# Optimization experiments

Measured on AMD Instinct MI355X. Metric: run time of the kernel, lower is better.

The kernel has to match this reference:

```python
import jax, jax.numpy as jnp
import numpy as np

IN_FEATURES = 4096
OUT_FEATURES = 4096
ACTIVE_IN = 1024
ACTIVE_OUT = 1024
BATCH, SEQ = 4, 2048


def setup_inputs() -> dict:
    key = jax.random.key(0)
    kx, kw, kb = jax.random.split(key, 3)
    x = jax.random.normal(kx, (BATCH, SEQ, IN_FEATURES), dtype=jnp.float32)
    # nn.Linear default init scale ~ 1/sqrt(fan_in)
    W = jax.random.normal(kw, (ACTIVE_OUT, ACTIVE_IN), dtype=jnp.float32) / np.sqrt(ACTIVE_IN)
    b = jax.random.normal(kb, (ACTIVE_OUT,), dtype=jnp.float32) / np.sqrt(ACTIVE_IN)
    rng = np.random.default_rng(42)
    # unique sorted index subsets (faithful to pruning-style selection; scatter is write-once)
    in_idx = jnp.asarray(np.sort(rng.choice(IN_FEATURES, ACTIVE_IN, replace=False)), dtype=jnp.int32)
    out_idx = jnp.asarray(np.sort(rng.choice(OUT_FEATURES, ACTIVE_OUT, replace=False)), dtype=jnp.int32)
    return {"x": x, "W": W, "b": b, "in_idx": in_idx, "out_idx": out_idx}


def reference(x, W, b, in_idx, out_idx):
    # gather active input columns: [B, S, ACTIVE_IN]
    x_active = jnp.take(x, in_idx, axis=-1)
    # dense linear: y = x_active @ W.T + b -> [B, S, ACTIVE_OUT]
    y = jnp.einsum('bsi,oi->bso', x_active, W) + b
    # scatter into zero-initialized full output buffer: [B, S, OUT_FEATURES]
    out = jnp.zeros(x.shape[:-1] + (OUT_FEATURES,), dtype=y.dtype)
    out = out.at[..., out_idx].set(y)
    return out
```

## Files before the change

### kernel.cpp

```cpp
#include <hip/hip_runtime.h>
#include <hip/hip_bf16.h>


typedef unsigned short u16;
typedef u16   u16x4 __attribute__((ext_vector_type(4)));
typedef int   i32x4 __attribute__((ext_vector_type(4)));
typedef float f32x4 __attribute__((ext_vector_type(4)));
typedef __bf16 bf16x8 __attribute__((ext_vector_type(8)));

constexpr int IN_F  = 4096;
constexpr int OUT_F = 4096;
constexpr int AI    = 1024;
constexpr int AO    = 1024;
constexpr int M_ROWS = 4 * 2048;

__device__ __forceinline__ u16 f2bf(float f) {
    union { __hip_bfloat16 h; u16 u; } cv;
    cv.h = __float2bfloat16(f);
    return cv.u;
}
__device__ __forceinline__ float bf2f(u16 u) {
    union { float f; unsigned int i; } cv;
    cv.i = ((unsigned int)u) << 16;
    return cv.f;
}

__global__ void prep_kernel(const float* __restrict__ W,
                            const int* __restrict__ out_idx,
                            u16* __restrict__ Wb, int* __restrict__ pos) {
    int t = blockIdx.x * blockDim.x + threadIdx.x;
    if (t < AO) pos[out_idx[t]] = t;
    f32x4 w = reinterpret_cast<const f32x4*>(W)[t];
    u16x4 v;
    v.x = f2bf(w.x); v.y = f2bf(w.y); v.z = f2bf(w.z); v.w = f2bf(w.w);
    reinterpret_cast<u16x4*>(Wb)[t] = v;
}

__global__ __launch_bounds__(256)
void gather_kernel(const float* __restrict__ x,
                   const int* __restrict__ in_idx,
                   u16* __restrict__ Xa) {
    __shared__ float xrow[IN_F];
    const int m = blockIdx.x;
    const int t = threadIdx.x;
    const f32x4* src = reinterpret_cast<const f32x4*>(x + (size_t)m * IN_F);
#pragma unroll
    for (int i = 0; i < 4; ++i)
        *reinterpret_cast<f32x4*>(&xrow[i * 1024 + t * 4]) = src[i * 256 + t];
    __syncthreads();
    i32x4 idx = reinterpret_cast<const i32x4*>(in_idx)[t];
    u16x4 v;
    v.x = f2bf(xrow[idx.x]);
    v.y = f2bf(xrow[idx.y]);
    v.z = f2bf(xrow[idx.z]);
    v.w = f2bf(xrow[idx.w]);
    reinterpret_cast<u16x4*>(Xa + (size_t)m * AI)[t] = v;
}

__global__ __launch_bounds__(256, 2)
void gemmfw_kernel(const u16* __restrict__ Xa, const u16* __restrict__ Wb,
                   const float* __restrict__ bias,
                   const int* __restrict__ out_idx,
                   const int* __restrict__ pos, float* __restrict__ out) {
    __shared__ u16 S[4][128 * 64];
    const int t    = threadIdx.x;
    const int wid  = t >> 6;
    const int lane = t & 63;
    const int n_lo = lane & 15;
    const int kg   = lane >> 4;
    const int orig = blockIdx.x;
    const int wgid = (orig & 7) * 64 + (orig >> 3);
    const int mb = wgid >> 3, nb = wgid & 7;
    const int m0 = mb * 128, n0 = nb * 128;
    const int wm = wid >> 1, wn = wid & 1;

    const int r8 = lane >> 3;
    const int c8 = (lane & 7) * 8;
    auto stage = [&](int buf, int k0) {
#pragma unroll
        for (int c = 0; c < 4; ++c) {
            const int row = wid * 32 + c * 8;
            __builtin_amdgcn_global_load_lds(
                (const __attribute__((address_space(1))) void*)
                    (Xa + (size_t)(m0 + row + r8) * AI + k0 + c8),
                (__attribute__((address_space(3))) void*)&S[buf][row * 64],
                16, 0, 0);
            __builtin_amdgcn_global_load_lds(
                (const __attribute__((address_space(1))) void*)
                    (Wb + (size_t)(n0 + row + r8) * AI + k0 + c8),
                (__attribute__((address_space(3))) void*)&S[2 + buf][row * 64],
                16, 0, 0);
        }
    };

    f32x4 acc[4][4];
#pragma unroll
    for (int i = 0; i < 4; ++i)
#pragma unroll
        for (int j = 0; j < 4; ++j) acc[i][j] = (f32x4)0.0f;

    stage(0, 0);
    int buf = 0;
    for (int kt = 0; kt < AI / 64; ++kt) {
        __syncthreads();
        if (kt + 1 < AI / 64) stage(buf ^ 1, (kt + 1) * 64);
#pragma unroll
        for (int kk = 0; kk < 64; kk += 32) {
            bf16x8 a[4], b[4];
#pragma unroll
            for (int i = 0; i < 4; ++i)
                a[i] = *reinterpret_cast<const bf16x8*>(
                    &S[buf][(wm * 64 + i * 16 + n_lo) * 64 + kk + kg * 8]);
#pragma unroll
            for (int j = 0; j < 4; ++j)
                b[j] = *reinterpret_cast<const bf16x8*>(
                    &S[2 + buf][(wn * 64 + j * 16 + n_lo) * 64 + kk + kg * 8]);
#pragma unroll
            for (int i = 0; i < 4; ++i)
#pragma unroll
                for (int j = 0; j < 4; ++j)
                    acc[i][j] = __builtin_amdgcn_mfma_f32_16x16x32_bf16(
                        a[i], b[j], acc[i][j], 0, 0, 0);
        }
        buf ^= 1;
    }

    float bv[4];
#pragma unroll
    for (int j = 0; j < 4; ++j) bv[j] = bias[n0 + wn * 64 + j * 16 + n_lo];

    __syncthreads();
    u16* ys = &S[0][0];
#pragma unroll
    for (int i = 0; i < 4; ++i)
#pragma unroll
        for (int j = 0; j < 4; ++j)
#pragma unroll
            for (int r = 0; r < 4; ++r)
                ys[(wm * 64 + i * 16 + kg * 4 + r) * 136 +
                   wn * 64 + j * 16 + n_lo] = f2bf(acc[i][j][r] + bv[j]);
    __syncthreads();

    const int lo = (nb == 0) ? 0 : out_idx[nb * 128];
    const int hi = (nb == 7) ? OUT_F : out_idx[(nb + 1) * 128];
    const int s4 = (lo + 3) >> 2;
    const int e4 = hi >> 2;
    const i32x4* pos4 = reinterpret_cast<const i32x4*>(pos);
    const int rg = t >> 5, j32 = t & 31;
#pragma unroll 1
    for (int rr = 0; rr < 128; rr += 8) {
        const int row = rr + rg;
        float* orow = out + (size_t)(m0 + row) * OUT_F;
        const u16* yr = ys + row * 136;
        for (int c = lo + j32; c < s4 * 4; c += 32) {
            int p = pos[c];
            orow[c] = (p >= 0) ? bf2f(yr[p - n0]) : 0.0f;
        }
        for (int c4 = s4 + j32; c4 < e4; c4 += 32) {
            i32x4 p = pos4[c4];
            f32x4 v;
            v.x = (p.x >= 0) ? bf2f(yr[p.x - n0]) : 0.0f;
            v.y = (p.y >= 0) ? bf2f(yr[p.y - n0]) : 0.0f;
            v.z = (p.z >= 0) ? bf2f(yr[p.z - n0]) : 0.0f;
            v.w = (p.w >= 0) ? bf2f(yr[p.w - n0]) : 0.0f;
            reinterpret_cast<f32x4*>(orow)[c4] = v;
        }
        for (int c = e4 * 4 + j32; c < hi; c += 32) {
            int p = pos[c];
            orow[c] = (p >= 0) ? bf2f(yr[p - n0]) : 0.0f;
        }
    }
}

extern "C" void kernel_launch(void* const* d_in, const int* in_sizes, int n_in,
                              void* d_out, int out_size, void* d_ws, size_t ws_size,
                              hipStream_t stream) {
    const float* x      = (const float*)d_in[0];
    const float* W      = (const float*)d_in[1];
    const float* b      = (const float*)d_in[2];
    const int*   in_idx = (const int*)d_in[3];
    const int*   out_idx= (const int*)d_in[4];
    float* out = (float*)d_out;

    char* ws = (char*)d_ws;
    int* pos = (int*)ws;
    u16* Wb  = (u16*)(ws + 16384);
    u16* Xa  = (u16*)(ws + 16384 + 2 * 1024 * 1024);

    hipMemsetAsync(pos, 0xFF, OUT_F * sizeof(int), stream);
    prep_kernel<<<1024, 256, 0, stream>>>(W, out_idx, Wb, pos);
    gather_kernel<<<M_ROWS, 256, 0, stream>>>(x, in_idx, Xa);
    gemmfw_kernel<<<(M_ROWS / 128) * (AO / 128), 256, 0, stream>>>(
        Xa, Wb, b, out_idx, pos, out);
}
```

Before: 286.6 us.

## Fuse weight prep into gather kernel and halve GEMM K-tile for occupancy

Folds the weight bf16 conversion and out_idx position-map build into the first 1024 blocks of the gather kernel, removing one kernel launch. The GEMM K-tile shrinks from 64 to 32, cutting LDS use from 64KB to about 34KB (sized by the epilogue staging buffer), and launch bounds rise to 4 blocks per SM to raise occupancy. In exchange the loop runs twice as many iterations with a barrier each, and there is less work per sync to hide load latency.

```diff
diff --git a/kernel.cpp b/kernel.cpp
--- a/kernel.cpp
+++ b/kernel.cpp
@@ -13,6 +13,8 @@
 constexpr int AI    = 1024;
 constexpr int AO    = 1024;
 constexpr int M_ROWS = 4 * 2048;
+constexpr int BK    = 32;
+constexpr int NKT   = AI / BK;
 
 __device__ __forceinline__ u16 f2bf(float f) {
     union { __hip_bfloat16 h; u16 u; } cv;
@@ -25,24 +27,24 @@
     return cv.f;
 }
 
-__global__ void prep_kernel(const float* __restrict__ W,
-                            const int* __restrict__ out_idx,
-                            u16* __restrict__ Wb, int* __restrict__ pos) {
-    int t = blockIdx.x * blockDim.x + threadIdx.x;
-    if (t < AO) pos[out_idx[t]] = t;
-    f32x4 w = reinterpret_cast<const f32x4*>(W)[t];
-    u16x4 v;
-    v.x = f2bf(w.x); v.y = f2bf(w.y); v.z = f2bf(w.z); v.w = f2bf(w.w);
-    reinterpret_cast<u16x4*>(Wb)[t] = v;
-}
-
 __global__ __launch_bounds__(256)
 void gather_kernel(const float* __restrict__ x,
                    const int* __restrict__ in_idx,
+                   const float* __restrict__ W,
+                   const int* __restrict__ out_idx,
+                   u16* __restrict__ Wb, int* __restrict__ pos,
                    u16* __restrict__ Xa) {
     __shared__ float xrow[IN_F];
     const int m = blockIdx.x;
     const int t = threadIdx.x;
+    if (m < 1024) {
+        const int t2 = m * 256 + t;
+        if (t2 < AO) pos[out_idx[t2]] = t2;
+        f32x4 w = reinterpret_cast<const f32x4*>(W)[t2];
+        u16x4 wv;
+        wv.x = f2bf(w.x); wv.y = f2bf(w.y); wv.z = f2bf(w.z); wv.w = f2bf(w.w);
+        reinterpret_cast<u16x4*>(Wb)[t2] = wv;
+    }
     const f32x4* src = reinterpret_cast<const f32x4*>(x + (size_t)m * IN_F);
 #pragma unroll
     for (int i = 0; i < 4; ++i)
@@ -57,12 +59,12 @@
     reinterpret_cast<u16x4*>(Xa + (size_t)m * AI)[t] = v;
 }
 
-__global__ __launch_bounds__(256, 2)
+__global__ __launch_bounds__(256, 4)
 void gemmfw_kernel(const u16* __restrict__ Xa, const u16* __restrict__ Wb,
                    const float* __restrict__ bias,
                    const int* __restrict__ out_idx,
                    const int* __restrict__ pos, float* __restrict__ out) {
-    __shared__ u16 S[4][128 * 64];
+    __shared__ char L[128 * 136 * 2];
     const int t    = threadIdx.x;
     const int wid  = t >> 6;
     const int lane = t & 63;
@@ -74,21 +76,22 @@
     const int m0 = mb * 128, n0 = nb * 128;
     const int wm = wid >> 1, wn = wid & 1;
 
-    const int r8 = lane >> 3;
-    const int c8 = (lane & 7) * 8;
+    const int r16 = lane >> 2;
+    const int c8  = (lane & 3) * 8;
     auto stage = [&](int buf, int k0) {
 #pragma unroll
-        for (int c = 0; c < 4; ++c) {
-            const int row = wid * 32 + c * 8;
+        for (int h = 0; h < 2; ++h) {
+            const int row = h * 64 + wid * 16 + r16;
+            const int db  = (h * 64 + wid * 16) * 64;
             __builtin_amdgcn_global_load_lds(
                 (const __attribute__((address_space(1))) void*)
-                    (Xa + (size_t)(m0 + row + r8) * AI + k0 + c8),
-                (__attribute__((address_space(3))) void*)&S[buf][row * 64],
+                    (Xa + (size_t)(m0 + row) * AI + k0 + c8),
+                (__attribute__((address_space(3))) void*)(L + buf * 8192 + db),
                 16, 0, 0);
             __builtin_amdgcn_global_load_lds(
                 (const __attribute__((address_space(1))) void*)
-                    (Wb + (size_t)(n0 + row + r8) * AI + k0 + c8),
-                (__attribute__((address_space(3))) void*)&S[2 + buf][row * 64],
+                    (Wb + (size_t)(n0 + row) * AI + k0 + c8),
+                (__attribute__((address_space(3))) void*)(L + 16384 + buf * 8192 + db),
                 16, 0, 0);
         }
     };
@@ -101,27 +104,24 @@
 
     stage(0, 0);
     int buf = 0;
-    for (int kt = 0; kt < AI / 64; ++kt) {
+    for (int kt = 0; kt < NKT; ++kt) {
         __syncthreads();
-        if (kt + 1 < AI / 64) stage(buf ^ 1, (kt + 1) * 64);
+        if (kt + 1 < NKT) stage(buf ^ 1, (kt + 1) * BK);
+        bf16x8 a[4], b[4];
 #pragma unroll
-        for (int kk = 0; kk < 64; kk += 32) {
-            bf16x8 a[4], b[4];
+        for (int i = 0; i < 4; ++i)
+            a[i] = *reinterpret_cast<const bf16x8*>(
+                L + buf * 8192 + (wm * 64 + i * 16 + n_lo) * 64 + kg * 16);
 #pragma unroll
-            for (int i = 0; i < 4; ++i)
-                a[i] = *reinterpret_cast<const bf16x8*>(
-                    &S[buf][(wm * 64 + i * 16 + n_lo) * 64 + kk + kg * 8]);
+        for (int j = 0; j < 4; ++j)
+            b[j] = *reinterpret_cast<const bf16x8*>(
+                L + 16384 + buf * 8192 + (wn * 64 + j * 16 + n_lo) * 64 + kg * 16);
+#pragma unroll
+        for (int i = 0; i < 4; ++i)
 #pragma unroll
             for (int j = 0; j < 4; ++j)
-                b[j] = *reinterpret_cast<const bf16x8*>(
-                    &S[2 + buf][(wn * 64 + j * 16 + n_lo) * 64 + kk + kg * 8]);
-#pragma unroll
-            for (int i = 0; i < 4; ++i)
-#pragma unroll
-                for (int j = 0; j < 4; ++j)
-                    acc[i][j] = __builtin_amdgcn_mfma_f32_16x16x32_bf16(
-                        a[i], b[j], acc[i][j], 0, 0, 0);
-        }
+                acc[i][j] = __builtin_amdgcn_mfma_f32_16x16x32_bf16(
+                    a[i], b[j], acc[i][j], 0, 0, 0);
         buf ^= 1;
     }
 
@@ -130,7 +130,7 @@
     for (int j = 0; j < 4; ++j) bv[j] = bias[n0 + wn * 64 + j * 16 + n_lo];
 
     __syncthreads();
-    u16* ys = &S[0][0];
+    u16* ys = reinterpret_cast<u16*>(L);
 #pragma unroll
     for (int i = 0; i < 4; ++i)
 #pragma unroll
@@ -188,8 +188,7 @@
     u16* Xa  = (u16*)(ws + 16384 + 2 * 1024 * 1024);
 
     hipMemsetAsync(pos, 0xFF, OUT_F * sizeof(int), stream);
-    prep_kernel<<<1024, 256, 0, stream>>>(W, out_idx, Wb, pos);
-    gather_kernel<<<M_ROWS, 256, 0, stream>>>(x, in_idx, Xa);
+    gather_kernel<<<M_ROWS, 256, 0, stream>>>(x, in_idx, W, out_idx, Wb, pos, Xa);
     gemmfw_kernel<<<(M_ROWS / 128) * (AO / 128), 256, 0, stream>>>(
         Xa, Wb, b, out_idx, pos, out);
 }
```

After: 281.5 us. About the same (-1.8%).
